# Optimization experiments

Measured on AMD Instinct MI355X. Metric: run time of the kernel, lower is better.

## Reference

```python
import jax, jax.numpy as jnp
import numpy as np

LN2 = float(np.log(2.0))
CUTOFF_L = 0.5


def _ssp(x):
    # shifted softplus: log(0.5*exp(x) + 0.5)
    return jax.nn.softplus(x) - LN2


def _pair_idx(n):
    # ordered pairs arranged [n, n-1]: for each i, all j != i
    idx = np.arange(n)
    j = np.stack([np.concatenate([idx[:k], idx[k + 1:]]) for k in range(n)])  # [n, n-1]
    i = np.broadcast_to(idx[:, None], j.shape)
    return jnp.asarray(i), jnp.asarray(j)


def _mlp3(x, w1, b1, w2, b2, w3, b3):
    h = _ssp(x @ w1 + b1)
    h = _ssp(h @ w2 + b2)
    return h @ w3 + b3


def _backflow_cutoff(r, L=CUTOFF_L):
    r = r / L
    return jnp.where(r < L, r ** 2 * (6.0 - 8.0 * r + 3.0 * r ** 2), jnp.ones((), r.dtype))


def setup_inputs() -> dict:
    key = jax.random.key(0)
    ks = jax.random.split(key, 12)
    B, N, D, K = 512, 32, 256, 8
    dims_e = [D, 40, 6, 1]
    dims_n = [D, 81, 25, 8]

    def lin(k, fi, fo):
        return jax.random.normal(k, (fi, fo), jnp.float32) / np.sqrt(fi)

    inp = {
        'rs': jax.random.normal(ks[0], (B, N, 3), jnp.float32),
        'xs': jax.random.normal(ks[1], (B, N, D), jnp.float32),
        'coords': jax.random.normal(ks[2], (K, 3), jnp.float32) * 2.0,
        'ew1': lin(ks[3], dims_e[0], dims_e[1]), 'eb1': jnp.zeros((dims_e[1],), jnp.float32),
        'ew2': lin(ks[4], dims_e[1], dims_e[2]), 'eb2': jnp.zeros((dims_e[2],), jnp.float32),
        'ew3': lin(ks[5], dims_e[2], dims_e[3]), 'eb3': jnp.zeros((dims_e[3],), jnp.float32),
        'nw1': lin(ks[6], dims_n[0], dims_n[1]), 'nb1': jnp.zeros((dims_n[1],), jnp.float32),
        'nw2': lin(ks[7], dims_n[1], dims_n[2]), 'nb2': jnp.zeros((dims_n[2],), jnp.float32),
        'nw3': lin(ks[8], dims_n[2], dims_n[3]), 'nb3': jnp.zeros((dims_n[3],), jnp.float32),
    }
    return inp


def reference(rs, xs, coords, ew1, eb1, ew2, eb2, ew3, eb3,
              nw1, nb1, nw2, nb2, nw3, nb3):
    n_elec = rs.shape[-2]
    i, j = _pair_idx(n_elec)  # [n, n-1] static index arrays

    # electron-electron backflow
    diffs_elec = rs[..., i, :] - rs[..., j, :]                    # [B, n, n-1, 3]
    pair_feat = xs[..., i, :] * xs[..., j, :]                     # [B, n, n-1, D]
    w_pair = _mlp3(pair_feat, ew1, eb1, ew2, eb2, ew3, eb3)       # [B, n, n-1, 1]
    bf_elec = (w_pair * diffs_elec).sum(axis=-2)                  # [B, n, 3]

    # electron-nucleus backflow
    diffs_nuc = rs[..., :, None, :] - coords                      # [B, n, K, 3]
    w_nuc = _mlp3(xs, nw1, nb1, nw2, nb2, nw3, nb3)               # [B, n, K]
    bf_nuc = (w_nuc[..., None] * diffs_nuc).sum(axis=-2)          # [B, n, 3]

    dist_nuc = jnp.linalg.norm(diffs_nuc, axis=-1)                # [B, n, K]
    cutoff = _backflow_cutoff(dist_nuc).prod(axis=-1)             # [B, n]

    return rs + 1e-4 * cutoff[..., None] * (bf_elec + bf_nuc)
```

## Files before the change

### kernel.cpp

```cpp
#include <hip/hip_runtime.h>
#include <stdint.h>

static constexpr int B_ = 512, N_ = 32, D_ = 256, K_ = 8;
static constexpr int E1 = 40, E2 = 6;
static constexpr int N1 = 81, N2 = 25, N3 = 8;
static constexpr int XBP = 264;
static constexpr int HEP = 104;
static constexpr int EWT = 264;
static constexpr int TKP = 40;
static constexpr int NWP = 104;
static constexpr int TILE16 = 16 * TKP;
static constexpr float LN2f  = 0.69314718055994530942f;
static constexpr float L2Ef  = 1.44269504088896340736f;

typedef float    f32x4 __attribute__((ext_vector_type(4)));
typedef _Float16 f16x8 __attribute__((ext_vector_type(8)));
typedef _Float16 f16x4 __attribute__((ext_vector_type(4)));

#if __has_builtin(__builtin_amdgcn_mfma_f32_16x16x16_f16)
#define MFMA16(A, B, C) __builtin_amdgcn_mfma_f32_16x16x16_f16((A), (B), (C), 0, 0, 0)
#else
#define MFMA16(A, B, C) __builtin_amdgcn_mfma_f32_16x16x16f16((A), (B), (C), 0, 0, 0)
#endif

__device__ __forceinline__ float ssp2(float t) {
    float e = __builtin_amdgcn_exp2f(t);
    return __builtin_amdgcn_logf(fmaf(e, 0.5f, 0.5f));
}

__global__ __launch_bounds__(512) void k_fused(
    const float* __restrict__ rs, const float* __restrict__ xs,
    const float* __restrict__ coords,
    const float* __restrict__ ew1, const float* __restrict__ eb1,
    const float* __restrict__ ew2, const float* __restrict__ eb2,
    const float* __restrict__ ew3, const float* __restrict__ eb3,
    const float* __restrict__ nw1, const float* __restrict__ nb1,
    const float* __restrict__ nw2, const float* __restrict__ nb2,
    const float* __restrict__ nw3, const float* __restrict__ nb3,
    float* __restrict__ out)
{
    __shared__ alignas(16) _Float16 xs_h[N_ * XBP];
    __shared__ alignas(16) _Float16 wbuf[E1 * EWT];
    __shared__ alignas(16) char uni[17664];
    __shared__ float nw3_s[N2 * N3];
    __shared__ float rs_s[N_ * 3];
    __shared__ float nb2_s[N2];
    __shared__ float nb3_s[N3];
    __shared__ float co_s[K_ * 3];
    __shared__ float bfn_s[N_ * 3];
    __shared__ float cut_s[N_];
    __shared__ float bfe_s[N_ * 3];
    __shared__ alignas(16) float eb1_s[48];
    __shared__ alignas(16) float b2_s[16];

    _Float16* h1e  = (_Float16*)(uni + 7680);
    float*    h2e  = (float*)(uni + 14336);
    _Float16* nw2T = (_Float16*)uni;

    const int b = blockIdx.x, t = threadIdx.x;
    const int wv = t >> 6, l = t & 63, quad = l >> 4, c = l & 15;

    f16x4 b2fT[3];
    #pragma unroll
    for (int Nt = 0; Nt < 3; ++Nt) {
        f16x4 p;
        #pragma unroll
        for (int r = 0; r < 4; ++r) {
            int n = Nt * 16 + quad * 4 + r;
            p[r] = (_Float16)((n < E1 && c < E2) ? ew2[n * E2 + c] : 0.f);
        }
        b2fT[Nt] = p;
    }
    float w3q[4];
    #pragma unroll
    for (int r = 0; r < 4; ++r) {
        int m = quad * 4 + r;
        w3q[r] = (m < E2) ? ew3[m] * LN2f : 0.f;
    }
    const float eb3v = eb3[0];

    {
        const float4* src = (const float4*)(xs + (size_t)b * N_ * D_);
        #pragma unroll
        for (int u = 0; u < 4; ++u) {
            int q = t + 512 * u;
            float4 v = src[q];
            int row = q >> 6, col4 = q & 63;
            union { _Float16 h[4]; uint64_t u64; } pk;
            pk.h[0] = (_Float16)v.x; pk.h[1] = (_Float16)v.y;
            pk.h[2] = (_Float16)v.z; pk.h[3] = (_Float16)v.w;
            *(uint64_t*)&xs_h[row * XBP + col4 * 4] = pk.u64;
        }
    }
    {
        const float4* src = (const float4*)ew1;
        #pragma unroll
        for (int u = 0; u < 5; ++u) {
            int q = t + 512 * u;
            float4 v = src[q];
            int k = q / 10, n0 = (q - 10 * k) * 4;
            wbuf[(n0 + 0) * EWT + k] = (_Float16)(v.x * L2Ef);
            wbuf[(n0 + 1) * EWT + k] = (_Float16)(v.y * L2Ef);
            wbuf[(n0 + 2) * EWT + k] = (_Float16)(v.z * L2Ef);
            wbuf[(n0 + 3) * EWT + k] = (_Float16)(v.w * L2Ef);
        }
    }
    if (t < 128) {
        int m = t >> 2, q4 = t & 3;
        *(uint64_t*)(uni + 7680 + m * (HEP * 2) + 160 + q4 * 8) = 0ull;
    }
    if (t < N_ * 3) rs_s[t] = rs[b * N_ * 3 + t];
    if (t < N2 * N3) nw3_s[t] = nw3[t] * LN2f;
    if (t < N2) nb2_s[t] = nb2[t] * L2Ef;
    if (t < N3) nb3_s[t] = nb3[t];
    if (t < K_ * 3) co_s[t] = coords[t];
    if (t < 48) eb1_s[t] = (t < E1) ? eb1[t] * L2Ef : 0.f;
    if (t < 16) b2_s[t] = (t < E2) ? eb2[t] * L2Ef : 0.f;
    __syncthreads();

    if (wv < 6) {
        _Float16* tile = (_Float16*)uni + wv * TILE16;
        const int ln = l & 15, lq = l >> 4;
        const int gn = wv * 16 + ln;
        const bool gok = (gn < N1);
        const int n_col = wv * 16 + c;
        const float nb1v = (n_col < N1) ? nb1[n_col] * L2Ef : 0.f;

        float pf[8];
        #pragma unroll
        for (int u = 0; u < 8; ++u)
            pf[u] = gok ? nw1[(lq + 4 * u) * N1 + gn] : 0.f;

        f32x4 acc[2];
        acc[0] = (f32x4){0.f, 0.f, 0.f, 0.f};
        acc[1] = (f32x4){0.f, 0.f, 0.f, 0.f};

        #pragma unroll 1
        for (int Kt = 0; Kt < 8; ++Kt) {
            #pragma unroll
            for (int u = 0; u < 8; ++u)
                tile[ln * TKP + lq + 4 * u] = (_Float16)(pf[u] * L2Ef);
            if (Kt < 7) {
                const float* wk = nw1 + (Kt + 1) * 32 * N1 + gn;
                #pragma unroll
                for (int u = 0; u < 8; ++u)
                    pf[u] = gok ? wk[(lq + 4 * u) * N1] : 0.f;
            }
            f16x8 Bf = *(const f16x8*)&tile[c * TKP + quad * 8];
            #pragma unroll
            for (int Mt = 0; Mt < 2; ++Mt) {
                f16x8 A = *(const f16x8*)&xs_h[(Mt * 16 + c) * XBP + Kt * 32 + quad * 8];
                acc[Mt] = __builtin_amdgcn_mfma_f32_16x16x32_f16(A, Bf, acc[Mt], 0, 0, 0);
            }
        }
        if (n_col < N1) {
            #pragma unroll
            for (int Mt = 0; Mt < 2; ++Mt)
                #pragma unroll
                for (int r2 = 0; r2 < 4; ++r2) {
                    int m = Mt * 16 + quad * 4 + r2;
                    h1e[m * HEP + n_col] = (_Float16)ssp2(acc[Mt][r2] + nb1v);
                }
        }
    }
    __syncthreads();

    f16x8 b1f[3][8];
    #pragma unroll
    for (int Nt = 0; Nt < 3; ++Nt) {
        int n = Nt * 16 + c;
        bool ok = (n < E1);
        int row = ok ? n : 0;
        #pragma unroll
        for (int Kt = 0; Kt < 8; ++Kt) {
            f16x8 v = *(const f16x8*)&wbuf[row * EWT + Kt * 32 + quad * 8];
            if (!ok) v = (f16x8)(_Float16)0.f;
            b1f[Nt][Kt] = v;
        }
    }
    #pragma unroll
    for (int u = 0; u < 6; ++u) {
        int idx = t + 512 * u;
        int n = idx / 96, kk = idx - 96 * n;
        float v = (kk < N1 && n < N2) ? nw2[kk * N2 + n] : 0.f;
        nw2T[n * NWP + kk] = (_Float16)v;
    }
    __syncthreads();

    if (wv < 4) {
        const int Mt = wv & 1, Nt = wv >> 1;
        f32x4 acc2 = {0.f, 0.f, 0.f, 0.f};
        #pragma unroll
        for (int Kt2 = 0; Kt2 < 3; ++Kt2) {
            f16x8 A  = *(const f16x8*)&h1e[(Mt * 16 + c) * HEP + Kt2 * 32 + quad * 8];
            f16x8 Bf = *(const f16x8*)&nw2T[(Nt * 16 + c) * NWP + Kt2 * 32 + quad * 8];
            acc2 = __builtin_amdgcn_mfma_f32_16x16x32_f16(A, Bf, acc2, 0, 0, 0);
        }
        int n = Nt * 16 + c;
        if (n < N2) {
            #pragma unroll
            for (int r2 = 0; r2 < 4; ++r2) {
                int m = Mt * 16 + quad * 4 + r2;
                h2e[m * 26 + n] = ssp2(acc2[r2] + nb2_s[n]);
            }
        }
    }
    __syncthreads();

    if (t < 256) {
        const int r = t >> 3, s = t & 7;
        float w = nb3_s[s];
        const int rb = r * 26;
        #pragma unroll
        for (int kk = 0; kk < N2; ++kk)
            w = fmaf(h2e[rb + kk], nw3_s[kk * N3 + s], w);

        float dx = rs_s[r * 3 + 0] - co_s[s * 3 + 0];
        float dy = rs_s[r * 3 + 1] - co_s[s * 3 + 1];
        float dz = rs_s[r * 3 + 2] - co_s[s * 3 + 2];
        float cx = w * dx, cy = w * dy, cz = w * dz;
        #pragma unroll
        for (int m2 = 1; m2 < 8; m2 <<= 1) {
            cx += __shfl_xor(cx, m2);
            cy += __shfl_xor(cy, m2);
            cz += __shfl_xor(cz, m2);
        }
        float rr  = sqrtf(dx * dx + dy * dy + dz * dz);
        float xsc = 2.f * rr;
        float cf  = (xsc < 0.5f) ? xsc * xsc * (6.f - 8.f * xsc + 3.f * xsc * xsc) : 1.f;
        #pragma unroll
        for (int m2 = 1; m2 < 8; m2 <<= 1) cf *= __shfl_xor(cf, m2);
        if (s == 0) {
            bfn_s[r * 3 + 0] = cx;
            bfn_s[r * 3 + 1] = cy;
            bfn_s[r * 3 + 2] = cz;
            cut_s[r] = cf;
        }
    }

    #pragma unroll 1
    for (int q8 = 0; q8 < 4; ++q8) {
        const int i = wv + 8 * q8;
        f32x4 acc[2][3];
        #pragma unroll
        for (int Nt = 0; Nt < 3; ++Nt) {
            f32x4 bias = *(const f32x4*)&eb1_s[Nt * 16 + quad * 4];
            acc[0][Nt] = bias;
            acc[1][Nt] = bias;
        }

        #pragma unroll
        for (int Kt = 0; Kt < 8; ++Kt) {
            const int koff = Kt * 32 + quad * 8;
            f16x8 iv  = *(const f16x8*)&xs_h[i * XBP + koff];
            f16x8 jv0 = *(const f16x8*)&xs_h[c * XBP + koff];
            f16x8 jv1 = *(const f16x8*)&xs_h[(16 + c) * XBP + koff];
            f16x8 P0 = iv * jv0;
            f16x8 P1 = iv * jv1;
            #pragma unroll
            for (int Nt = 0; Nt < 3; ++Nt) {
                acc[0][Nt] = __builtin_amdgcn_mfma_f32_16x16x32_f16(b1f[Nt][Kt], P0, acc[0][Nt], 0, 0, 0);
                acc[1][Nt] = __builtin_amdgcn_mfma_f32_16x16x32_f16(b1f[Nt][Kt], P1, acc[1][Nt], 0, 0, 0);
            }
        }

        const float rix = rs_s[i * 3 + 0], riy = rs_s[i * 3 + 1], riz = rs_s[i * 3 + 2];
        float cxi = 0.f, cyi = 0.f, czi = 0.f;
        const f32x4 b2i = *(const f32x4*)&b2_s[quad * 4];
        #pragma unroll
        for (int h = 0; h < 2; ++h) {
            f32x4 acc2 = b2i;
            #pragma unroll
            for (int Nt = 0; Nt < 3; ++Nt) {
                f16x4 bh;
                #pragma unroll
                for (int r2 = 0; r2 < 4; ++r2)
                    bh[r2] = (_Float16)ssp2(acc[h][Nt][r2]);
                acc2 = MFMA16(b2fT[Nt], bh, acc2);
            }
            float ws = 0.f;
            #pragma unroll
            for (int r2 = 0; r2 < 4; ++r2)
                ws = fmaf(w3q[r2], ssp2(acc2[r2]), ws);
            ws += __shfl_xor(ws, 16);
            ws += __shfl_xor(ws, 32);
            float wj = ws + eb3v;
            int j = c + 16 * h;
            cxi = fmaf(wj, rix - rs_s[j * 3 + 0], cxi);
            cyi = fmaf(wj, riy - rs_s[j * 3 + 1], cyi);
            czi = fmaf(wj, riz - rs_s[j * 3 + 2], czi);
        }
        #pragma unroll
        for (int m2 = 1; m2 < 16; m2 <<= 1) {
            cxi += __shfl_xor(cxi, m2);
            cyi += __shfl_xor(cyi, m2);
            czi += __shfl_xor(czi, m2);
        }
        if (l == 0) {
            bfe_s[i * 3 + 0] = cxi;
            bfe_s[i * 3 + 1] = cyi;
            bfe_s[i * 3 + 2] = czi;
        }
    }
    __syncthreads();

    if (t < N_ * 3) {
        int i = t / 3;
        out[(size_t)b * (N_ * 3) + t] =
            rs_s[t] + 1e-4f * cut_s[i] * (bfe_s[t] + bfn_s[t]);
    }
}

extern "C" void kernel_launch(void* const* d_in, const int* in_sizes, int n_in,
                              void* d_out, int out_size, void* d_ws, size_t ws_size,
                              hipStream_t stream)
{
    const float* rs     = (const float*)d_in[0];
    const float* xs     = (const float*)d_in[1];
    const float* coords = (const float*)d_in[2];
    const float* ew1    = (const float*)d_in[3];
    const float* eb1    = (const float*)d_in[4];
    const float* ew2    = (const float*)d_in[5];
    const float* eb2    = (const float*)d_in[6];
    const float* ew3    = (const float*)d_in[7];
    const float* eb3    = (const float*)d_in[8];
    const float* nw1    = (const float*)d_in[9];
    const float* nb1    = (const float*)d_in[10];
    const float* nw2    = (const float*)d_in[11];
    const float* nb2    = (const float*)d_in[12];
    const float* nw3    = (const float*)d_in[13];
    const float* nb3    = (const float*)d_in[14];

    k_fused<<<B_, 512, 0, stream>>>(rs, xs, coords, ew1, eb1, ew2, eb2, ew3, eb3,
                                    nw1, nb1, nw2, nb2, nw3, nb3, (float*)d_out);
}
```

Before: 129.5 us.

## Process two electrons per wave iteration and stream ew1 fragments from LDS

The pair-MLP main loop now handles two i-electrons per iteration (iA, iB), sharing the j-row loads and each ew1 fragment across four MFMAs instead of two. The ew1 fragments are no longer held in 48 f16x8 registers; they are re-read from LDS each Kt step, and the padding rows are zeroed so no masking is needed. This lowers register pressure and raises MFMA reuse per weight load, at the cost of more LDS reads and a larger live accumulator set.

```diff
diff --git a/kernel.cpp b/kernel.cpp
--- a/kernel.cpp
+++ b/kernel.cpp
@@ -27,6 +27,47 @@
     float e = __builtin_amdgcn_exp2f(t);
     return __builtin_amdgcn_logf(fmaf(e, 0.5f, 0.5f));
 }
+
+#define EE_EPI(ACC, I)                                                         \
+    {                                                                          \
+        const float rix = rs_s[(I) * 3 + 0], riy = rs_s[(I) * 3 + 1],          \
+                    riz = rs_s[(I) * 3 + 2];                                   \
+        float cxi = 0.f, cyi = 0.f, czi = 0.f;                                 \
+        _Pragma("unroll")                                                      \
+        for (int h = 0; h < 2; ++h) {                                          \
+            f32x4 acc2 = b2i;                                                  \
+            _Pragma("unroll")                                                  \
+            for (int Nt = 0; Nt < 3; ++Nt) {                                   \
+                f16x4 bh;                                                      \
+                _Pragma("unroll")                                              \
+                for (int r2 = 0; r2 < 4; ++r2)                                 \
+                    bh[r2] = (_Float16)ssp2(ACC[h][Nt][r2]);                   \
+                acc2 = MFMA16(b2fT[Nt], bh, acc2);                             \
+            }                                                                  \
+            float ws = 0.f;                                                    \
+            _Pragma("unroll")                                                  \
+            for (int r2 = 0; r2 < 4; ++r2)                                     \
+                ws = fmaf(w3q[r2], ssp2(acc2[r2]), ws);                        \
+            ws += __shfl_xor(ws, 16);                                          \
+            ws += __shfl_xor(ws, 32);                                          \
+            float wj = ws + eb3v;                                              \
+            int j = c + 16 * h;                                                \
+            cxi = fmaf(wj, rix - rs_s[j * 3 + 0], cxi);                        \
+            cyi = fmaf(wj, riy - rs_s[j * 3 + 1], cyi);                        \
+            czi = fmaf(wj, riz - rs_s[j * 3 + 2], czi);                        \
+        }                                                                      \
+        _Pragma("unroll")                                                      \
+        for (int m2 = 1; m2 < 16; m2 <<= 1) {                                  \
+            cxi += __shfl_xor(cxi, m2);                                        \
+            cyi += __shfl_xor(cyi, m2);                                        \
+            czi += __shfl_xor(czi, m2);                                        \
+        }                                                                      \
+        if (l == 0) {                                                          \
+            bfe_s[(I) * 3 + 0] = cxi;                                          \
+            bfe_s[(I) * 3 + 1] = cyi;                                          \
+            bfe_s[(I) * 3 + 2] = czi;                                          \
+        }                                                                      \
+    }
 
 __global__ __launch_bounds__(512) void k_fused(
     const float* __restrict__ rs, const float* __restrict__ xs,
@@ -40,7 +81,7 @@
     float* __restrict__ out)
 {
     __shared__ alignas(16) _Float16 xs_h[N_ * XBP];
-    __shared__ alignas(16) _Float16 wbuf[E1 * EWT];
+    __shared__ alignas(16) _Float16 wbuf[48 * EWT];
     __shared__ alignas(16) char uni[17664];
     __shared__ float nw3_s[N2 * N3];
     __shared__ float rs_s[N_ * 3];
@@ -105,6 +146,14 @@
             wbuf[(n0 + 3) * EWT + k] = (_Float16)(v.w * L2Ef);
         }
     }
+    {
+        uint32_t* z = (uint32_t*)(wbuf + 40 * EWT);
+        #pragma unroll
+        for (int u = 0; u < 3; ++u) {
+            int idx = t + 512 * u;
+            if (idx < 1056) z[idx] = 0u;
+        }
+    }
     if (t < 128) {
         int m = t >> 2, q4 = t & 3;
         *(uint64_t*)(uni + 7680 + m * (HEP * 2) + 160 + q4 * 8) = 0ull;
@@ -165,19 +214,6 @@
     }
     __syncthreads();
 
-    f16x8 b1f[3][8];
-    #pragma unroll
-    for (int Nt = 0; Nt < 3; ++Nt) {
-        int n = Nt * 16 + c;
-        bool ok = (n < E1);
-        int row = ok ? n : 0;
-        #pragma unroll
-        for (int Kt = 0; Kt < 8; ++Kt) {
-            f16x8 v = *(const f16x8*)&wbuf[row * EWT + Kt * 32 + quad * 8];
-            if (!ok) v = (f16x8)(_Float16)0.f;
-            b1f[Nt][Kt] = v;
-        }
-    }
     #pragma unroll
     for (int u = 0; u < 6; ++u) {
         int idx = t + 512 * u;
@@ -238,69 +274,38 @@
         }
     }
 
+    const f32x4 b2i = *(const f32x4*)&b2_s[quad * 4];
     #pragma unroll 1
-    for (int q8 = 0; q8 < 4; ++q8) {
-        const int i = wv + 8 * q8;
-        f32x4 acc[2][3];
+    for (int p = 0; p < 2; ++p) {
+        const int iA = wv + 16 * p, iB = iA + 8;
+        f32x4 accA[2][3], accB[2][3];
         #pragma unroll
         for (int Nt = 0; Nt < 3; ++Nt) {
             f32x4 bias = *(const f32x4*)&eb1_s[Nt * 16 + quad * 4];
-            acc[0][Nt] = bias;
-            acc[1][Nt] = bias;
+            accA[0][Nt] = bias; accA[1][Nt] = bias;
+            accB[0][Nt] = bias; accB[1][Nt] = bias;
         }
 
         #pragma unroll
         for (int Kt = 0; Kt < 8; ++Kt) {
             const int koff = Kt * 32 + quad * 8;
-            f16x8 iv  = *(const f16x8*)&xs_h[i * XBP + koff];
             f16x8 jv0 = *(const f16x8*)&xs_h[c * XBP + koff];
             f16x8 jv1 = *(const f16x8*)&xs_h[(16 + c) * XBP + koff];
-            f16x8 P0 = iv * jv0;
-            f16x8 P1 = iv * jv1;
+            f16x8 ivA = *(const f16x8*)&xs_h[iA * XBP + koff];
+            f16x8 ivB = *(const f16x8*)&xs_h[iB * XBP + koff];
+            f16x8 PA0 = ivA * jv0, PA1 = ivA * jv1;
+            f16x8 PB0 = ivB * jv0, PB1 = ivB * jv1;
             #pragma unroll
             for (int Nt = 0; Nt < 3; ++Nt) {
-                acc[0][Nt] = __builtin_amdgcn_mfma_f32_16x16x32_f16(b1f[Nt][Kt], P0, acc[0][Nt], 0, 0, 0);
-                acc[1][Nt] = __builtin_amdgcn_mfma_f32_16x16x32_f16(b1f[Nt][Kt], P1, acc[1][Nt], 0, 0, 0);
+                f16x8 Af = *(const f16x8*)&wbuf[(Nt * 16 + c) * EWT + koff];
+                accA[0][Nt] = __builtin_amdgcn_mfma_f32_16x16x32_f16(Af, PA0, accA[0][Nt], 0, 0, 0);
+                accA[1][Nt] = __builtin_amdgcn_mfma_f32_16x16x32_f16(Af, PA1, accA[1][Nt], 0, 0, 0);
+                accB[0][Nt] = __builtin_amdgcn_mfma_f32_16x16x32_f16(Af, PB0, accB[0][Nt], 0, 0, 0);
+                accB[1][Nt] = __builtin_amdgcn_mfma_f32_16x16x32_f16(Af, PB1, accB[1][Nt], 0, 0, 0);
             }
         }
-
-        const float rix = rs_s[i * 3 + 0], riy = rs_s[i * 3 + 1], riz = rs_s[i * 3 + 2];
-        float cxi = 0.f, cyi = 0.f, czi = 0.f;
-        const f32x4 b2i = *(const f32x4*)&b2_s[quad * 4];
-        #pragma unroll
-        for (int h = 0; h < 2; ++h) {
-            f32x4 acc2 = b2i;
-            #pragma unroll
-            for (int Nt = 0; Nt < 3; ++Nt) {
-                f16x4 bh;
-                #pragma unroll
-                for (int r2 = 0; r2 < 4; ++r2)
-                    bh[r2] = (_Float16)ssp2(acc[h][Nt][r2]);
-                acc2 = MFMA16(b2fT[Nt], bh, acc2);
-            }
-            float ws = 0.f;
-            #pragma unroll
-            for (int r2 = 0; r2 < 4; ++r2)
-                ws = fmaf(w3q[r2], ssp2(acc2[r2]), ws);
-            ws += __shfl_xor(ws, 16);
-            ws += __shfl_xor(ws, 32);
-            float wj = ws + eb3v;
-            int j = c + 16 * h;
-            cxi = fmaf(wj, rix - rs_s[j * 3 + 0], cxi);
-            cyi = fmaf(wj, riy - rs_s[j * 3 + 1], cyi);
-            czi = fmaf(wj, riz - rs_s[j * 3 + 2], czi);
-        }
-        #pragma unroll
-        for (int m2 = 1; m2 < 16; m2 <<= 1) {
-            cxi += __shfl_xor(cxi, m2);
-            cyi += __shfl_xor(cyi, m2);
-            czi += __shfl_xor(czi, m2);
-        }
-        if (l == 0) {
-            bfe_s[i * 3 + 0] = cxi;
-            bfe_s[i * 3 + 1] = cyi;
-            bfe_s[i * 3 + 2] = czi;
-        }
+        EE_EPI(accA, iA)
+        EE_EPI(accB, iB)
     }
     __syncthreads();
 
```

New measurement: 130.5 us. Within noise of the previous version (+0.8%).
